# Optimization experiments

Hardware: AMD Instinct MI355X
Metric: run time of the kernel (lower is better)

The kernel has to match this reference:

```python
import jax, jax.numpy as jnp
import numpy as np

H = 16
D_MODEL = 1024
D_K = D_MODEL // H
B, S = 4, 2048


def setup_inputs() -> dict:
    key = jax.random.key(0)
    ks = jax.random.split(key, 12)
    scale = 1.0 / np.sqrt(D_MODEL)
    inp = {
        "q": jax.random.normal(ks[0], (B, S, D_MODEL), dtype=jnp.float32),
        "k": jax.random.normal(ks[1], (B, S, D_MODEL), dtype=jnp.float32),
        "v": jax.random.normal(ks[2], (B, S, D_MODEL), dtype=jnp.float32),
        # torch nn.Linear weights: shape (out, in), y = x @ W.T + b
        "Wq": jax.random.uniform(ks[3], (D_MODEL, D_MODEL), minval=-scale, maxval=scale),
        "bq": jax.random.uniform(ks[4], (D_MODEL,), minval=-scale, maxval=scale),
        "Wk": jax.random.uniform(ks[5], (D_MODEL, D_MODEL), minval=-scale, maxval=scale),
        "bk": jax.random.uniform(ks[6], (D_MODEL,), minval=-scale, maxval=scale),
        "Wv": jax.random.uniform(ks[7], (D_MODEL, D_MODEL), minval=-scale, maxval=scale),
        "bv": jax.random.uniform(ks[8], (D_MODEL,), minval=-scale, maxval=scale),
        "Wo": jax.random.uniform(ks[9], (D_MODEL, D_MODEL), minval=-scale, maxval=scale),
        "bo": jax.random.uniform(ks[10], (D_MODEL,), minval=-scale, maxval=scale),
        "ln_g": jnp.ones((D_MODEL,), dtype=jnp.float32),
        "ln_b": jnp.zeros((D_MODEL,), dtype=jnp.float32),
    }
    return inp


def _layernorm(x, g, b, eps=1e-5):
    mu = jnp.mean(x, axis=-1, keepdims=True)
    var = jnp.var(x, axis=-1, keepdims=True)
    return (x - mu) * jax.lax.rsqrt(var + eps) * g + b


def reference(q, k, v, Wq, bq, Wk, bk, Wv, bv, Wo, bo, ln_g, ln_b):
    nb = q.shape[0]
    # projections, split heads -> (B, H, S, d_k)
    def proj(x, W, b):
        y = x @ W.T + b
        return y.reshape(nb, -1, H, D_K).transpose(0, 2, 1, 3)

    Q = proj(q, Wq, bq)
    K = proj(k, Wk, bk)
    V = proj(v, Wv, bv)

    scores = jnp.einsum("bhqd,bhkd->bhqk", Q, K) / jnp.sqrt(jnp.float32(D_K))
    p_attn = jax.nn.softmax(scores, axis=-1)
    x = jnp.einsum("bhqk,bhkd->bhqd", p_attn, V)
    x = x.transpose(0, 2, 1, 3).reshape(nb, -1, H * D_K)
    out = _layernorm(x @ Wo.T + bo + q, ln_g, ln_b)
    return out
```

## Files before the change

kernel.cpp:

```cpp
#include <hip/hip_runtime.h>

#define DM 1024
#define NH 16
#define DK 64
#define SEQ 2048
#define BATCH 4
#define M_TOT (BATCH * SEQ)

typedef short s16x8 __attribute__((ext_vector_type(8)));
typedef float f32x4 __attribute__((ext_vector_type(4)));
typedef unsigned int u32x4 __attribute__((ext_vector_type(4)));
typedef unsigned int u32x2 __attribute__((ext_vector_type(2)));

#define MFMA16(a, b, c) __builtin_amdgcn_mfma_f32_16x16x32_bf16((a), (b), (c), 0, 0, 0)

#define QSCALE 0.1803368801111244f

__device__ __forceinline__ float bf2f(unsigned short u) {
    return __uint_as_float(((unsigned int)u) << 16);
}
__device__ __forceinline__ unsigned short f2bf(float f) {
    unsigned int u = __float_as_uint(f);
    u += 0x7FFFu + ((u >> 16) & 1u);
    return (unsigned short)(u >> 16);
}
__device__ __forceinline__ unsigned int pack_bf2(unsigned int lo, unsigned int hi) {
    return ((lo + 0x8000u) >> 16) | ((hi + 0x8000u) & 0xFFFF0000u);
}
__device__ __forceinline__ unsigned int pack_bf2_trunc(float lo, float hi) {
    return __builtin_amdgcn_perm(__float_as_uint(hi), __float_as_uint(lo), 0x07060302u);
}
__device__ __forceinline__ s16x8 load_cvt8(const float* p) {
    u32x4 x0 = *reinterpret_cast<const u32x4*>(p);
    u32x4 x1 = *reinterpret_cast<const u32x4*>(p + 4);
    union { s16x8 v; unsigned int u[4]; } r;
    r.u[0] = pack_bf2(x0[0], x0[1]);
    r.u[1] = pack_bf2(x0[2], x0[3]);
    r.u[2] = pack_bf2(x1[0], x1[1]);
    r.u[3] = pack_bf2(x1[2], x1[3]);
    return r.v;
}

__device__ __forceinline__ void ld_lds16(const unsigned short* g, unsigned short* lds_base) {
    __builtin_amdgcn_global_load_lds(
        (const __attribute__((address_space(1))) unsigned int*)g,
        (__attribute__((address_space(3))) unsigned int*)lds_base,
        16, 0, 0);
}

__global__ __launch_bounds__(256) void cvt_bf16_kernel(
    const float* __restrict__ src, unsigned short* __restrict__ dst, int n)
{
    const int i = (blockIdx.x * 256 + threadIdx.x) * 8;
    if (i >= n) return;
    *reinterpret_cast<s16x8*>(dst + i) = load_cvt8(src + i);
}

__global__ __launch_bounds__(256) void cvt_w_kernel(
    const float* __restrict__ w0, const float* __restrict__ w1,
    const float* __restrict__ w2, const float* __restrict__ w3,
    unsigned short* __restrict__ dst)
{
    const float* src = blockIdx.y == 0 ? w0 : blockIdx.y == 1 ? w1
                     : blockIdx.y == 2 ? w2 : w3;
    const long off = (long)blockIdx.y * ((long)DM * DM);
    const int i = (blockIdx.x * 256 + threadIdx.x) * 8;
    *reinterpret_cast<s16x8*>(dst + off + i) = load_cvt8(src + i);
}

__global__ __launch_bounds__(256) void gemm_kernel(
    const unsigned short* __restrict__ Ab,
    const unsigned short* __restrict__ Wb,
    const float* __restrict__ bias,
    unsigned short* __restrict__ Y,
    const int mode, const float scale)
{
    const int tid  = threadIdx.x;
    const int lane = tid & 63;
    const int wave = tid >> 6;
    const int c16  = lane & 15;
    const int quad = lane >> 4;
    const int m0 = blockIdx.x * 128;
    const int n0 = blockIdx.y * 128;
    const int wm = (wave >> 1) * 64;
    const int wn = (wave & 1) * 64;

    __shared__ __align__(16) unsigned short As[128 * 32];
    __shared__ __align__(16) unsigned short Bs[128 * 32];

    f32x4 acc[4][4];
    #pragma unroll
    for (int tm = 0; tm < 4; ++tm)
        #pragma unroll
        for (int tn = 0; tn < 4; ++tn) acc[tm][tn] = (f32x4){0.f, 0.f, 0.f, 0.f};

    int srow[2], sch[2];
    #pragma unroll
    for (int c = 0; c < 2; ++c) {
        const int s = c * 256 + wave * 64 + lane;
        srow[c] = s >> 2;
        sch[c]  = s & 3;
    }

    for (int k0 = 0; k0 < DM; k0 += 32) {
        #pragma unroll
        for (int c = 0; c < 2; ++c) {
            unsigned short* abase = As + (c * 256 + wave * 64) * 8;
            unsigned short* bbase = Bs + (c * 256 + wave * 64) * 8;
            ld_lds16(Ab + (long)(m0 + srow[c]) * DM + k0 + sch[c] * 8, abase);
            ld_lds16(Wb + (long)(n0 + srow[c]) * DM + k0 + sch[c] * 8, bbase);
        }
        __syncthreads();

        s16x8 a[4], b[4];
        #pragma unroll
        for (int tm = 0; tm < 4; ++tm)
            a[tm] = *reinterpret_cast<const s16x8*>(As + (wm + tm * 16 + c16) * 32 + quad * 8);
        #pragma unroll
        for (int tn = 0; tn < 4; ++tn)
            b[tn] = *reinterpret_cast<const s16x8*>(Bs + (wn + tn * 16 + c16) * 32 + quad * 8);
        #pragma unroll
        for (int tm = 0; tm < 4; ++tm)
            #pragma unroll
            for (int tn = 0; tn < 4; ++tn)
                acc[tm][tn] = MFMA16(a[tm], b[tn], acc[tm][tn]);
        __syncthreads();
    }

    #pragma unroll
    for (int tn = 0; tn < 4; ++tn) {
        const int col = n0 + wn + tn * 16 + c16;
        const float bv = bias[col];
        const int h = col >> 6, d = col & 63;
        #pragma unroll
        for (int tm = 0; tm < 4; ++tm) {
            #pragma unroll
            for (int r = 0; r < 4; ++r) {
                const int m = m0 + wm + tm * 16 + quad * 4 + r;
                const int b_ = m >> 11;
                const int s  = m & 2047;
                const float v = (acc[tm][tn][r] + bv) * scale;
                long idx;
                if (mode == 0)      idx = (((long)(b_ * NH + h) * SEQ + s) * DK) + d;
                else if (mode == 1) idx = (((long)(b_ * NH + h) * DK + d) * SEQ) + s;
                else                idx = (long)m * DM + col;
                Y[idx] = f2bf(v);
            }
        }
    }
}

__global__ __launch_bounds__(256, 4) void attn_kernel(
    const unsigned short* __restrict__ Qh,
    const unsigned short* __restrict__ Kh,
    const unsigned short* __restrict__ Vt,
    unsigned short* __restrict__ Xo)
{
    const int lane = threadIdx.x & 63;
    const int wave = threadIdx.x >> 6;
    const int c16  = lane & 15;
    const int quad = lane >> 4;
    const int bh = blockIdx.x;
    const int b_ = bh >> 4, h = bh & 15;
    const int m0 = blockIdx.y * 128 + wave * 32;

    __shared__ __align__(16) unsigned short Ks[2 * 64 * 64];
    __shared__ __align__(16) unsigned short Vs[2 * 64 * 64];

    const unsigned short* Kbh = Kh + (long)bh * SEQ * DK;
    const unsigned short* Vbh = Vt + (long)bh * DK * SEQ;

    s16x8 bQ[2][2];
    #pragma unroll
    for (int qt = 0; qt < 2; ++qt) {
        const unsigned short* qb = Qh + ((long)bh * SEQ + m0 + qt * 16 + c16) * DK + quad * 8;
        bQ[qt][0] = *reinterpret_cast<const s16x8*>(qb);
        bQ[qt][1] = *reinterpret_cast<const s16x8*>(qb + 32);
    }

    f32x4 o[2][4];
    #pragma unroll
    for (int qt = 0; qt < 2; ++qt)
        #pragma unroll
        for (int c = 0; c < 4; ++c) o[qt][c] = (f32x4){0.f, 0.f, 0.f, 0.f};
    float li[2] = {0.f, 0.f};

    int st_n[4], st_x[4], st_isK[4];
    #pragma unroll
    for (int j = 0; j < 4; ++j) {
        const int c = wave * 4 + j;
        const int s = (c & 7) * 64 + lane;
        st_isK[j] = (c < 8);
        st_n[j] = s >> 3;
        st_x[j] = (s & 7) ^ (st_n[j] & 7);
    }

    auto stage = [&](int buf, int n0) {
        #pragma unroll
        for (int j = 0; j < 4; ++j) {
            const int c = wave * 4 + j;
            if (st_isK[j])
                ld_lds16(Kbh + (n0 + st_n[j]) * DK + st_x[j] * 8,
                         &Ks[buf * 4096 + (c & 7) * 512]);
            else
                ld_lds16(Vbh + (long)st_n[j] * SEQ + n0 + st_x[j] * 8,
                         &Vs[buf * 4096 + (c & 7) * 512]);
        }
    };

    stage(0, 0);
    __syncthreads();

    for (int it = 0; it < SEQ / 64; ++it) {
        const int cur = it & 1;
        if (it + 1 < SEQ / 64) stage(cur ^ 1, (it + 1) * 64);

        const unsigned short* Kb = Ks + cur * 4096;
        const unsigned short* Vb = Vs + cur * 4096;

        f32x4 st[2][4];
        #pragma unroll
        for (int t = 0; t < 4; ++t) {
            const int n = t * 16 + c16;
            const int sw = n & 7;
            s16x8 a0 = *reinterpret_cast<const s16x8*>(&Kb[n * 64 + ((quad ^ sw) * 8)]);
            s16x8 a1 = *reinterpret_cast<const s16x8*>(&Kb[n * 64 + (((quad + 4) ^ sw) * 8)]);
            #pragma unroll
            for (int qt = 0; qt < 2; ++qt) {
                f32x4 s = (f32x4){0.f, 0.f, 0.f, 0.f};
                s = MFMA16(a0, bQ[qt][0], s);
                s = MFMA16(a1, bQ[qt][1], s);
                st[qt][t] = s;
            }
        }

        s16x8 bP[2][2];
        #pragma unroll
        for (int qt = 0; qt < 2; ++qt) {
            float psum = 0.f;
            #pragma unroll
            for (int t = 0; t < 4; ++t)
                #pragma unroll
                for (int r = 0; r < 4; ++r) {
                    const float p = exp2f(st[qt][t][r]);
                    st[qt][t][r] = p;
                    psum += p;
                }
            li[qt] += psum;

            uint2 w[4];
            #pragma unroll
            for (int t = 0; t < 4; ++t) {
                w[t].x = pack_bf2_trunc(st[qt][t][0], st[qt][t][1]);
                w[t].y = pack_bf2_trunc(st[qt][t][2], st[qt][t][3]);
            }
            #pragma unroll
            for (int hh = 0; hh < 2; ++hh) {
                u32x2 s0 = __builtin_amdgcn_permlane32_swap(w[2 * hh].x, w[2 * hh + 1].x, false, false);
                u32x2 s1 = __builtin_amdgcn_permlane32_swap(w[2 * hh].y, w[2 * hh + 1].y, false, false);
                u32x2 t0 = __builtin_amdgcn_permlane16_swap(s0[0], s0[1], false, false);
                u32x2 t1 = __builtin_amdgcn_permlane16_swap(s1[0], s1[1], false, false);
                union { s16x8 v; unsigned int u[4]; } f;
                f.u[0] = t0[0];
                f.u[1] = t1[0];
                f.u[2] = t0[1];
                f.u[3] = t1[1];
                bP[qt][hh] = f.v;
            }
        }

        #pragma unroll
        for (int cc = 0; cc < 4; ++cc) {
            const int d = cc * 16 + c16;
            const int sw = d & 7;
            s16x8 a0 = *reinterpret_cast<const s16x8*>(&Vb[d * 64 + ((quad ^ sw) * 8)]);
            s16x8 a1 = *reinterpret_cast<const s16x8*>(&Vb[d * 64 + (((quad + 4) ^ sw) * 8)]);
            #pragma unroll
            for (int qt = 0; qt < 2; ++qt) {
                o[qt][cc] = MFMA16(a0, bP[qt][0], o[qt][cc]);
                o[qt][cc] = MFMA16(a1, bP[qt][1], o[qt][cc]);
            }
        }
        __syncthreads();
    }

    #pragma unroll
    for (int qt = 0; qt < 2; ++qt) {
        float l = li[qt];
        l += __shfl_xor(l, 16, 64);
        l += __shfl_xor(l, 32, 64);
        const float inv = 1.f / l;
        unsigned short* orow = Xo + ((long)b_ * SEQ + m0 + qt * 16 + c16) * DM + h * DK;
        #pragma unroll
        for (int c = 0; c < 4; ++c) {
            uint2 w;
            w.x = pack_bf2(__float_as_uint(o[qt][c][0] * inv), __float_as_uint(o[qt][c][1] * inv));
            w.y = pack_bf2(__float_as_uint(o[qt][c][2] * inv), __float_as_uint(o[qt][c][3] * inv));
            *reinterpret_cast<uint2*>(orow + c * 16 + quad * 4) = w;
        }
    }
}

__global__ __launch_bounds__(256) void ln_kernel(
    const unsigned short* __restrict__ Xlin,
    const float* __restrict__ qres,
    const float* __restrict__ g,
    const float* __restrict__ bb,
    float* __restrict__ out)
{
    const int row = blockIdx.x;
    const int tid = threadIdx.x;
    const int c0 = tid * 4;
    const int lane = tid & 63, wave = tid >> 6;

    __shared__ float ssum[4], ssq[4];

    uint2 xb = *reinterpret_cast<const uint2*>(Xlin + (long)row * DM + c0);
    float4 qv = *reinterpret_cast<const float4*>(qres + (long)row * DM + c0);
    float v[4];
    v[0] = bf2f((unsigned short)(xb.x & 0xFFFF)) + qv.x;
    v[1] = bf2f((unsigned short)(xb.x >> 16))    + qv.y;
    v[2] = bf2f((unsigned short)(xb.y & 0xFFFF)) + qv.z;
    v[3] = bf2f((unsigned short)(xb.y >> 16))    + qv.w;

    float s = v[0] + v[1] + v[2] + v[3];
    float q2 = v[0]*v[0] + v[1]*v[1] + v[2]*v[2] + v[3]*v[3];
    #pragma unroll
    for (int d = 1; d < 64; d <<= 1) {
        s  += __shfl_xor(s, d, 64);
        q2 += __shfl_xor(q2, d, 64);
    }
    if (lane == 0) { ssum[wave] = s; ssq[wave] = q2; }
    __syncthreads();
    const float ts = ssum[0] + ssum[1] + ssum[2] + ssum[3];
    const float tq = ssq[0] + ssq[1] + ssq[2] + ssq[3];
    const float mu = ts * (1.f / 1024.f);
    const float var = tq * (1.f / 1024.f) - mu * mu;
    const float rstd = rsqrtf(var + 1e-5f);

    float4 gv = *reinterpret_cast<const float4*>(g + c0);
    float4 bv = *reinterpret_cast<const float4*>(bb + c0);
    float4 o;
    o.x = (v[0] - mu) * rstd * gv.x + bv.x;
    o.y = (v[1] - mu) * rstd * gv.y + bv.y;
    o.z = (v[2] - mu) * rstd * gv.z + bv.z;
    o.w = (v[3] - mu) * rstd * gv.w + bv.w;
    *reinterpret_cast<float4*>(out + (long)row * DM + c0) = o;
}

extern "C" void kernel_launch(void* const* d_in, const int* in_sizes, int n_in,
                              void* d_out, int out_size, void* d_ws, size_t ws_size,
                              hipStream_t stream) {
    const float* q   = (const float*)d_in[0];
    const float* k   = (const float*)d_in[1];
    const float* v   = (const float*)d_in[2];
    const float* Wq  = (const float*)d_in[3];
    const float* bq  = (const float*)d_in[4];
    const float* Wk  = (const float*)d_in[5];
    const float* bk  = (const float*)d_in[6];
    const float* Wv  = (const float*)d_in[7];
    const float* bvv = (const float*)d_in[8];
    const float* Wo  = (const float*)d_in[9];
    const float* bo  = (const float*)d_in[10];
    const float* lng = (const float*)d_in[11];
    const float* lnb = (const float*)d_in[12];

    unsigned short* ws = (unsigned short*)d_ws;
    const long WE = (long)DM * DM;
    const long NE = (long)M_TOT * DM;
    unsigned short* Wqb = ws;
    unsigned short* Wkb = Wqb + WE;
    unsigned short* Wvb = Wkb + WE;
    unsigned short* Wob = Wvb + WE;
    unsigned short* U1  = Wob + WE;
    unsigned short* U2  = U1 + NE;
    unsigned short* U3  = U2 + NE;
    unsigned short* U4  = U3 + NE;

    dim3 blk(256);
    const int cvtW = (int)(WE / 2048);
    const int cvtX = (int)(NE / 2048);
    cvt_w_kernel<<<dim3(cvtW, 4), blk, 0, stream>>>(Wq, Wk, Wv, Wo, Wqb);

    dim3 ggemm(M_TOT / 128, DM / 128);
    cvt_bf16_kernel<<<cvtX, blk, 0, stream>>>(q, U1, (int)NE);
    gemm_kernel<<<ggemm, blk, 0, stream>>>(U1, Wqb, bq, U2, 0, QSCALE);
    cvt_bf16_kernel<<<cvtX, blk, 0, stream>>>(k, U1, (int)NE);
    gemm_kernel<<<ggemm, blk, 0, stream>>>(U1, Wkb, bk, U3, 0, 1.0f);
    cvt_bf16_kernel<<<cvtX, blk, 0, stream>>>(v, U1, (int)NE);
    gemm_kernel<<<ggemm, blk, 0, stream>>>(U1, Wvb, bvv, U4, 1, 1.0f);

    attn_kernel<<<dim3(BATCH * NH, SEQ / 128), blk, 0, stream>>>(U2, U3, U4, U1);

    gemm_kernel<<<ggemm, blk, 0, stream>>>(U1, Wob, bo, U2, 2, 1.0f);
    ln_kernel<<<dim3(M_TOT), blk, 0, stream>>>(U2, q, lng, lnb, (float*)d_out);
}
```

Measured before the change: 417.3 us.

## Halve attention query tile, drop LDS double buffer, raise occupancy with setprio

Each wave of the attention kernel now handles 16 query rows instead of 32, so each block covers 64 rows and the grid doubles. The K/V LDS staging goes from double-buffered to single-buffered with a sync after each load, and launch bounds are raised to 8 blocks per CU. s_setprio is raised around the MFMA sections. The aim is higher occupancy and lower register and LDS pressure so that wave switching hides latency. In exchange, K/V loads are no longer overlapped with compute inside a block, and each K/V tile is read from global memory twice as often in total.

```diff
diff --git a/kernel.cpp b/kernel.cpp
--- a/kernel.cpp
+++ b/kernel.cpp
@@ -150,7 +150,7 @@
     }
 }
 
-__global__ __launch_bounds__(256, 4) void attn_kernel(
+__global__ __launch_bounds__(256, 8) void attn_kernel(
     const unsigned short* __restrict__ Qh,
     const unsigned short* __restrict__ Kh,
     const unsigned short* __restrict__ Vt,
@@ -162,28 +162,25 @@
     const int quad = lane >> 4;
     const int bh = blockIdx.x;
     const int b_ = bh >> 4, h = bh & 15;
-    const int m0 = blockIdx.y * 128 + wave * 32;
-
-    __shared__ __align__(16) unsigned short Ks[2 * 64 * 64];
-    __shared__ __align__(16) unsigned short Vs[2 * 64 * 64];
+    const int m0 = blockIdx.y * 64 + wave * 16;
+
+    __shared__ __align__(16) unsigned short Ks[64 * 64];
+    __shared__ __align__(16) unsigned short Vs[64 * 64];
 
     const unsigned short* Kbh = Kh + (long)bh * SEQ * DK;
     const unsigned short* Vbh = Vt + (long)bh * DK * SEQ;
 
-    s16x8 bQ[2][2];
-    #pragma unroll
-    for (int qt = 0; qt < 2; ++qt) {
-        const unsigned short* qb = Qh + ((long)bh * SEQ + m0 + qt * 16 + c16) * DK + quad * 8;
-        bQ[qt][0] = *reinterpret_cast<const s16x8*>(qb);
-        bQ[qt][1] = *reinterpret_cast<const s16x8*>(qb + 32);
-    }
-
-    f32x4 o[2][4];
-    #pragma unroll
-    for (int qt = 0; qt < 2; ++qt)
-        #pragma unroll
-        for (int c = 0; c < 4; ++c) o[qt][c] = (f32x4){0.f, 0.f, 0.f, 0.f};
-    float li[2] = {0.f, 0.f};
+    s16x8 bQ[2];
+    {
+        const unsigned short* qb = Qh + ((long)bh * SEQ + m0 + c16) * DK + quad * 8;
+        bQ[0] = *reinterpret_cast<const s16x8*>(qb);
+        bQ[1] = *reinterpret_cast<const s16x8*>(qb + 32);
+    }
+
+    f32x4 o[4];
+    #pragma unroll
+    for (int c = 0; c < 4; ++c) o[c] = (f32x4){0.f, 0.f, 0.f, 0.f};
+    float li = 0.f;
 
     int st_n[4], st_x[4], st_isK[4];
     #pragma unroll
@@ -195,109 +192,91 @@
         st_x[j] = (s & 7) ^ (st_n[j] & 7);
     }
 
-    auto stage = [&](int buf, int n0) {
+    for (int n0 = 0; n0 < SEQ; n0 += 64) {
         #pragma unroll
         for (int j = 0; j < 4; ++j) {
             const int c = wave * 4 + j;
             if (st_isK[j])
-                ld_lds16(Kbh + (n0 + st_n[j]) * DK + st_x[j] * 8,
-                         &Ks[buf * 4096 + (c & 7) * 512]);
+                ld_lds16(Kbh + (n0 + st_n[j]) * DK + st_x[j] * 8, &Ks[(c & 7) * 512]);
             else
-                ld_lds16(Vbh + (long)st_n[j] * SEQ + n0 + st_x[j] * 8,
-                         &Vs[buf * 4096 + (c & 7) * 512]);
-        }
-    };
-
-    stage(0, 0);
-    __syncthreads();
-
-    for (int it = 0; it < SEQ / 64; ++it) {
-        const int cur = it & 1;
-        if (it + 1 < SEQ / 64) stage(cur ^ 1, (it + 1) * 64);
-
-        const unsigned short* Kb = Ks + cur * 4096;
-        const unsigned short* Vb = Vs + cur * 4096;
-
-        f32x4 st[2][4];
+                ld_lds16(Vbh + (long)st_n[j] * SEQ + n0 + st_x[j] * 8, &Vs[(c & 7) * 512]);
+        }
+        __syncthreads();
+
+        f32x4 st[4];
+        __builtin_amdgcn_s_setprio(1);
         #pragma unroll
         for (int t = 0; t < 4; ++t) {
             const int n = t * 16 + c16;
             const int sw = n & 7;
-            s16x8 a0 = *reinterpret_cast<const s16x8*>(&Kb[n * 64 + ((quad ^ sw) * 8)]);
-            s16x8 a1 = *reinterpret_cast<const s16x8*>(&Kb[n * 64 + (((quad + 4) ^ sw) * 8)]);
+            s16x8 a0 = *reinterpret_cast<const s16x8*>(&Ks[n * 64 + ((quad ^ sw) * 8)]);
+            s16x8 a1 = *reinterpret_cast<const s16x8*>(&Ks[n * 64 + (((quad + 4) ^ sw) * 8)]);
+            f32x4 s = (f32x4){0.f, 0.f, 0.f, 0.f};
+            s = MFMA16(a0, bQ[0], s);
+            s = MFMA16(a1, bQ[1], s);
+            st[t] = s;
+        }
+        __builtin_amdgcn_s_setprio(0);
+
+        #pragma unroll
+        for (int t = 0; t < 4; ++t)
             #pragma unroll
-            for (int qt = 0; qt < 2; ++qt) {
-                f32x4 s = (f32x4){0.f, 0.f, 0.f, 0.f};
-                s = MFMA16(a0, bQ[qt][0], s);
-                s = MFMA16(a1, bQ[qt][1], s);
-                st[qt][t] = s;
-            }
-        }
-
-        s16x8 bP[2][2];
-        #pragma unroll
-        for (int qt = 0; qt < 2; ++qt) {
-            float psum = 0.f;
-            #pragma unroll
-            for (int t = 0; t < 4; ++t)
-                #pragma unroll
-                for (int r = 0; r < 4; ++r) {
-                    const float p = exp2f(st[qt][t][r]);
-                    st[qt][t][r] = p;
-                    psum += p;
-                }
-            li[qt] += psum;
-
-            uint2 w[4];
-            #pragma unroll
-            for (int t = 0; t < 4; ++t) {
-                w[t].x = pack_bf2_trunc(st[qt][t][0], st[qt][t][1]);
-                w[t].y = pack_bf2_trunc(st[qt][t][2], st[qt][t][3]);
-            }
-            #pragma unroll
-            for (int hh = 0; hh < 2; ++hh) {
-                u32x2 s0 = __builtin_amdgcn_permlane32_swap(w[2 * hh].x, w[2 * hh + 1].x, false, false);
-                u32x2 s1 = __builtin_amdgcn_permlane32_swap(w[2 * hh].y, w[2 * hh + 1].y, false, false);
-                u32x2 t0 = __builtin_amdgcn_permlane16_swap(s0[0], s0[1], false, false);
-                u32x2 t1 = __builtin_amdgcn_permlane16_swap(s1[0], s1[1], false, false);
-                union { s16x8 v; unsigned int u[4]; } f;
-                f.u[0] = t0[0];
-                f.u[1] = t1[0];
-                f.u[2] = t0[1];
-                f.u[3] = t1[1];
-                bP[qt][hh] = f.v;
-            }
-        }
-
+            for (int r = 0; r < 4; ++r)
+                st[t][r] = exp2f(st[t][r]);
+        {
+            float t0 = (st[0][0] + st[0][1]) + (st[0][2] + st[0][3]);
+            float t1 = (st[1][0] + st[1][1]) + (st[1][2] + st[1][3]);
+            float t2 = (st[2][0] + st[2][1]) + (st[2][2] + st[2][3]);
+            float t3 = (st[3][0] + st[3][1]) + (st[3][2] + st[3][3]);
+            li += (t0 + t1) + (t2 + t3);
+        }
+
+        uint2 w[4];
+        #pragma unroll
+        for (int t = 0; t < 4; ++t) {
+            w[t].x = pack_bf2_trunc(st[t][0], st[t][1]);
+            w[t].y = pack_bf2_trunc(st[t][2], st[t][3]);
+        }
+        s16x8 bP[2];
+        #pragma unroll
+        for (int hh = 0; hh < 2; ++hh) {
+            u32x2 s0 = __builtin_amdgcn_permlane32_swap(w[2 * hh].x, w[2 * hh + 1].x, false, false);
+            u32x2 s1 = __builtin_amdgcn_permlane32_swap(w[2 * hh].y, w[2 * hh + 1].y, false, false);
+            u32x2 t0 = __builtin_amdgcn_permlane16_swap(s0[0], s0[1], false, false);
+            u32x2 t1 = __builtin_amdgcn_permlane16_swap(s1[0], s1[1], false, false);
+            union { s16x8 v; unsigned int u[4]; } f;
+            f.u[0] = t0[0];
+            f.u[1] = t1[0];
+            f.u[2] = t0[1];
+            f.u[3] = t1[1];
+            bP[hh] = f.v;
+        }
+
+        __builtin_amdgcn_s_setprio(1);
         #pragma unroll
         for (int cc = 0; cc < 4; ++cc) {
             const int d = cc * 16 + c16;
             const int sw = d & 7;
-            s16x8 a0 = *reinterpret_cast<const s16x8*>(&Vb[d * 64 + ((quad ^ sw) * 8)]);
-            s16x8 a1 = *reinterpret_cast<const s16x8*>(&Vb[d * 64 + (((quad + 4) ^ sw) * 8)]);
-            #pragma unroll
-            for (int qt = 0; qt < 2; ++qt) {
-                o[qt][cc] = MFMA16(a0, bP[qt][0], o[qt][cc]);
-                o[qt][cc] = MFMA16(a1, bP[qt][1], o[qt][cc]);
-            }
-        }
+            s16x8 a0 = *reinterpret_cast<const s16x8*>(&Vs[d * 64 + ((quad ^ sw) * 8)]);
+            s16x8 a1 = *reinterpret_cast<const s16x8*>(&Vs[d * 64 + (((quad + 4) ^ sw) * 8)]);
+            o[cc] = MFMA16(a0, bP[0], o[cc]);
+            o[cc] = MFMA16(a1, bP[1], o[cc]);
+        }
+        __builtin_amdgcn_s_setprio(0);
         __syncthreads();
     }
 
-    #pragma unroll
-    for (int qt = 0; qt < 2; ++qt) {
-        float l = li[qt];
-        l += __shfl_xor(l, 16, 64);
-        l += __shfl_xor(l, 32, 64);
-        const float inv = 1.f / l;
-        unsigned short* orow = Xo + ((long)b_ * SEQ + m0 + qt * 16 + c16) * DM + h * DK;
-        #pragma unroll
-        for (int c = 0; c < 4; ++c) {
-            uint2 w;
-            w.x = pack_bf2(__float_as_uint(o[qt][c][0] * inv), __float_as_uint(o[qt][c][1] * inv));
-            w.y = pack_bf2(__float_as_uint(o[qt][c][2] * inv), __float_as_uint(o[qt][c][3] * inv));
-            *reinterpret_cast<uint2*>(orow + c * 16 + quad * 4) = w;
-        }
+    float l = li;
+    l += __shfl_xor(l, 16, 64);
+    l += __shfl_xor(l, 32, 64);
+    const float inv = 1.f / l;
+    unsigned short* orow = Xo + ((long)b_ * SEQ + m0 + c16) * DM + h * DK;
+    #pragma unroll
+    for (int c = 0; c < 4; ++c) {
+        uint2 w;
+        w.x = pack_bf2(__float_as_uint(o[c][0] * inv), __float_as_uint(o[c][1] * inv));
+        w.y = pack_bf2(__float_as_uint(o[c][2] * inv), __float_as_uint(o[c][3] * inv));
+        *reinterpret_cast<uint2*>(orow + c * 16 + quad * 4) = w;
     }
 }
 
@@ -390,7 +369,7 @@
     cvt_bf16_kernel<<<cvtX, blk, 0, stream>>>(v, U1, (int)NE);
     gemm_kernel<<<ggemm, blk, 0, stream>>>(U1, Wvb, bvv, U4, 1, 1.0f);
 
-    attn_kernel<<<dim3(BATCH * NH, SEQ / 128), blk, 0, stream>>>(U2, U3, U4, U1);
+    attn_kernel<<<dim3(BATCH * NH, SEQ / 64), blk, 0, stream>>>(U2, U3, U4, U1);
 
     gemm_kernel<<<ggemm, blk, 0, stream>>>(U1, Wob, bo, U2, 2, 1.0f);
     ln_kernel<<<dim3(M_TOT), blk, 0, stream>>>(U2, q, lng, lnb, (float*)d_out);
```

Measured after the change: 520.2 us. 24.7% more time.
